# Kernel optimization log

Hardware: AMD Instinct MI355X
Metric: run time of the kernel (lower is better)

## Reference

```python
import jax, jax.numpy as jnp
import numpy as np
import functools

ISOVALUE = 0.0
OFFSET = 0.3  # quad half-extent used by the CPU fallback


def setup_inputs() -> dict:
    key = jax.random.key(0)
    k1, k2 = jax.random.split(key)
    grid = jax.random.normal(k1, (128, 128, 128), dtype=jnp.float32)
    deform = jax.random.normal(k2, (128, 128, 128, 3), dtype=jnp.float32)
    return {"grid": grid, "deform": deform}


def _mc_fallback(grid, deform):
    # Faithful, vectorized version of UniversalDiffMC.forward with the pure-CPU
    # fallback backend. Because JAX requires static shapes, we emit the dense
    # per-cell vertex/triangle buffers plus a validity mask instead of
    # compacting (inactive entries are zeroed).
    dimX, dimY, dimZ = grid.shape
    # F.pad(grid, (1,)*6, value=isovalue+1)
    gp = jnp.pad(grid, 1, constant_values=ISOVALUE + 1.0)        # [X+2,Y+2,Z+2]
    dp = jnp.pad(deform, ((1, 1), (1, 1), (1, 1), (0, 0)))       # [X+2,Y+2,Z+2,3]
    nx, ny, nz = dimX + 1, dimY + 1, dimZ + 1                    # cells of padded grid

    # 8 cube-corner values per cell via shifted slices
    def corner(dx, dy, dz):
        return gp[dx:dx + nx, dy:dy + ny, dz:dz + nz]
    corners = [corner(dx, dy, dz) for dx in (0, 1) for dy in (0, 1) for dz in (0, 1)]
    cmin = functools.reduce(jnp.minimum, corners)
    cmax = functools.reduce(jnp.maximum, corners)
    active = (cmin <= ISOVALUE) & (ISOVALUE <= cmax)             # [nx,ny,nz]

    # cell centers (x+0.5, y+0.5, z+0.5) + deform lookup at int(center)
    ix = jnp.arange(nx, dtype=grid.dtype)
    iy = jnp.arange(ny, dtype=grid.dtype)
    iz = jnp.arange(nz, dtype=grid.dtype)
    idx = jnp.stack(jnp.meshgrid(ix, iy, iz, indexing='ij'), axis=-1)  # [nx,ny,nz,3]
    center = idx + 0.5 + dp[:nx, :ny, :nz, :]                    # int(x+0.5)=x

    offs = jnp.array([[-OFFSET, -OFFSET, 0.0],
                      [ OFFSET, -OFFSET, 0.0],
                      [ OFFSET,  OFFSET, 0.0],
                      [-OFFSET,  OFFSET, 0.0]], dtype=grid.dtype)
    verts = center[..., None, :] + offs                          # [nx,ny,nz,4,3]
    verts = verts.reshape(-1, 3)

    # post-processing from forward(): shift back by padding, normalize to [-1,1)
    dims = jnp.array([dimX, dimY, dimZ], dtype=grid.dtype)
    verts = (verts - 1.0) / dims - 1.0

    mask_flat = active.reshape(-1)                                # [Ncells]
    vmask = jnp.repeat(mask_flat, 4)                              # [Ncells*4]
    verts = verts * vmask[:, None].astype(grid.dtype)

    ncells = nx * ny * nz
    base = jnp.arange(ncells, dtype=jnp.int32) * 4
    tri_pat = jnp.array([[0, 1, 2], [0, 2, 3]], dtype=jnp.int32)
    tris = (base[:, None, None] + tri_pat[None]).reshape(-1, 3)   # [Ncells*2,3]
    tmask = jnp.repeat(mask_flat, 2)
    tris = tris * tmask[:, None].astype(jnp.int32)
    return verts, tris, vmask


def reference(grid, deform):
    return _mc_fallback(grid, deform)
```

## Files before the change

kernel.cpp:

```cpp
#include <hip/hip_runtime.h>
#include <stdint.h>

constexpr int DIM    = 128;
constexpr int NCX    = 129;
constexpr int NCELLS = NCX * NCX * NCX;
constexpr size_t NV_ELEMS = (size_t)NCELLS * 12;
constexpr size_t NT_ELEMS = (size_t)NCELLS * 6;

constexpr int BLK = 256;

__device__ __forceinline__ float2 tri_pair(const float* __restrict__ smm,
                                           int c0, int j) {
    int cl = j / 3;
    int s  = j - 3 * cl;
    float mm = smm[cl];
    int base = (c0 + cl) * 4;
    int a = (s == 0) ? 0 : 2;
    int b = (s == 0) ? 1 : ((s == 1) ? 0 : 3);
    return make_float2((float)(base + a) * mm, (float)(base + b) * mm);
}

__global__ __launch_bounds__(BLK) void mc_kernel(
    const float* __restrict__ grid,
    const float* __restrict__ deform,
    float*       __restrict__ out)
{
    __shared__ __align__(16) float sv[BLK * 12];
    __shared__ float smm[BLK];

    const int t    = threadIdx.x;
    const int c0   = blockIdx.x * BLK;
    const int cell = c0 + t;

    if (cell < NCELLS) {
        int z  = cell % NCX;
        int tt = cell / NCX;
        int y  = tt % NCX;
        int x  = tt / NCX;

        float cmin = 3.4e38f, cmax = -3.4e38f;
        #pragma unroll
        for (int dx = 0; dx < 2; ++dx) {
            int i = x + dx - 1;
            bool iok = (unsigned)i < (unsigned)DIM;
            #pragma unroll
            for (int dy = 0; dy < 2; ++dy) {
                int j = y + dy - 1;
                bool jok = (unsigned)j < (unsigned)DIM;
                #pragma unroll
                for (int dz = 0; dz < 2; ++dz) {
                    int k = z + dz - 1;
                    bool kok = (unsigned)k < (unsigned)DIM;
                    float v = 1.0f;
                    if (iok && jok && kok)
                        v = grid[((size_t)i * DIM + j) * DIM + k];
                    cmin = fminf(cmin, v);
                    cmax = fmaxf(cmax, v);
                }
            }
        }
        float m = ((cmin <= 0.0f) && (cmax >= 0.0f)) ? 1.0f : 0.0f;

        float d0 = 0.f, d1 = 0.f, d2 = 0.f;
        {
            int i = x - 1, j = y - 1, k = z - 1;
            if ((unsigned)i < (unsigned)DIM && (unsigned)j < (unsigned)DIM &&
                (unsigned)k < (unsigned)DIM) {
                const float* b = deform + (((size_t)i * DIM + j) * DIM + k) * 3;
                d0 = b[0]; d1 = b[1]; d2 = b[2];
            }
        }
        float cx = (float)x + 0.5f + d0;
        float cy = (float)y + 0.5f + d1;
        float cz = (float)z + 0.5f + d2;

        constexpr float S = 1.0f / 128.0f;
        constexpr float B = -(1.0f / 128.0f) - 1.0f;
        float ax = fmaf(cx - 0.3f, S, B) * m;
        float bx = fmaf(cx + 0.3f, S, B) * m;
        float ay = fmaf(cy - 0.3f, S, B) * m;
        float by = fmaf(cy + 0.3f, S, B) * m;
        float gz = fmaf(cz,        S, B) * m;

        float4* v4 = reinterpret_cast<float4*>(sv) + t * 3;
        v4[0] = make_float4(ax, ay, gz, bx);
        v4[1] = make_float4(ay, gz, bx, by);
        v4[2] = make_float4(gz, ax, by, gz);

        smm[t] = m;
    }

    __syncthreads();

    float4*       gv  = reinterpret_cast<float4*>(out + (size_t)c0 * 12);
    const float4* lv  = reinterpret_cast<const float4*>(sv);
    float4*       gt4 = reinterpret_cast<float4*>(out + NV_ELEMS + (size_t)c0 * 6);
    float2*       gm  = reinterpret_cast<float2*>(out + NV_ELEMS + NT_ELEMS + (size_t)c0 * 4);

    if (c0 + BLK <= NCELLS) {
        #pragma unroll
        for (int r = 0; r < 3; ++r) gv[t + r * BLK] = lv[t + r * BLK];

        {
            float2 lo = tri_pair(smm, c0, 2 * t);
            float2 hi = tri_pair(smm, c0, 2 * t + 1);
            gt4[t] = make_float4(lo.x, lo.y, hi.x, hi.y);
            if (t < BLK / 2) {
                int p = BLK + t;
                float2 lo2 = tri_pair(smm, c0, 2 * p);
                float2 hi2 = tri_pair(smm, c0, 2 * p + 1);
                gt4[p] = make_float4(lo2.x, lo2.y, hi2.x, hi2.y);
            }
        }

        #pragma unroll
        for (int r = 0; r < 2; ++r) {
            int g = t + r * BLK;
            float mm = smm[g >> 1];
            gm[g] = make_float2(mm, mm);
        }
    } else {
        const int n = NCELLS - c0;
        for (int i = t; i < n * 3; i += BLK) gv[i] = lv[i];
        float2* gt2 = reinterpret_cast<float2*>(out + NV_ELEMS + (size_t)c0 * 6);
        for (int j = t; j < n * 3; j += BLK) gt2[j] = tri_pair(smm, c0, j);
        for (int g = t; g < n * 2; g += BLK) {
            float mm = smm[g >> 1];
            gm[g] = make_float2(mm, mm);
        }
    }
}

extern "C" void kernel_launch(void* const* d_in, const int* in_sizes, int n_in,
                              void* d_out, int out_size, void* d_ws, size_t ws_size,
                              hipStream_t stream) {
    const float* grid   = (const float*)d_in[0];
    const float* deform = (const float*)d_in[1];
    float* out = (float*)d_out;

    int blocks = (NCELLS + BLK - 1) / BLK;
    mc_kernel<<<blocks, BLK, 0, stream>>>(grid, deform, out);
}
```

Baseline: 39.94 us.

## Split vertex, triangle and mask output writes into separate block groups

The single kernel now dispatches three groups of blocks by block index: one writes vertices, one writes triangle indices, and one writes the vertex mask. The triangle and mask groups each recompute the cell activity mask from the grid. The aim is more blocks in flight, with each block writing one contiguous output region. The cost is that the 8-corner grid reads and min/max are done up to three times per cell.

```diff
diff --git a/kernel.cpp b/kernel.cpp
--- a/kernel.cpp
+++ b/kernel.cpp
@@ -8,6 +8,38 @@
 constexpr size_t NT_ELEMS = (size_t)NCELLS * 6;
 
 constexpr int BLK = 256;
+constexpr int NBV = (NCELLS + BLK - 1) / BLK;
+constexpr int NBT = NBV;
+constexpr int NBM = (NCELLS + 2 * BLK - 1) / (2 * BLK);
+
+__device__ __forceinline__ float cell_mask(const float* __restrict__ grid, int cell) {
+    int z  = cell % NCX;
+    int tt = cell / NCX;
+    int y  = tt % NCX;
+    int x  = tt / NCX;
+    float cmin = 3.4e38f, cmax = -3.4e38f;
+    #pragma unroll
+    for (int dx = 0; dx < 2; ++dx) {
+        int i = x + dx - 1;
+        bool iok = (unsigned)i < (unsigned)DIM;
+        #pragma unroll
+        for (int dy = 0; dy < 2; ++dy) {
+            int j = y + dy - 1;
+            bool jok = (unsigned)j < (unsigned)DIM;
+            #pragma unroll
+            for (int dz = 0; dz < 2; ++dz) {
+                int k = z + dz - 1;
+                bool kok = (unsigned)k < (unsigned)DIM;
+                float v = 1.0f;
+                if (iok && jok && kok)
+                    v = grid[((size_t)i * DIM + j) * DIM + k];
+                cmin = fminf(cmin, v);
+                cmax = fmaxf(cmax, v);
+            }
+        }
+    }
+    return ((cmin <= 0.0f) && (cmax >= 0.0f)) ? 1.0f : 0.0f;
+}
 
 __device__ __forceinline__ float2 tri_pair(const float* __restrict__ smm,
                                            int c0, int j) {
@@ -25,108 +57,102 @@
     const float* __restrict__ deform,
     float*       __restrict__ out)
 {
-    __shared__ __align__(16) float sv[BLK * 12];
-    __shared__ float smm[BLK];
+    __shared__ __align__(16) float sbuf[BLK * 12];
+    const int bid = blockIdx.x;
+    const int t   = threadIdx.x;
 
-    const int t    = threadIdx.x;
-    const int c0   = blockIdx.x * BLK;
-    const int cell = c0 + t;
+    if (bid < NBV) {
+        const int c0   = bid * BLK;
+        const int cell = c0 + t;
+        if (cell < NCELLS) {
+            int z  = cell % NCX;
+            int tt = cell / NCX;
+            int y  = tt % NCX;
+            int x  = tt / NCX;
+            float m = cell_mask(grid, cell);
 
-    if (cell < NCELLS) {
-        int z  = cell % NCX;
-        int tt = cell / NCX;
-        int y  = tt % NCX;
-        int x  = tt / NCX;
-
-        float cmin = 3.4e38f, cmax = -3.4e38f;
-        #pragma unroll
-        for (int dx = 0; dx < 2; ++dx) {
-            int i = x + dx - 1;
-            bool iok = (unsigned)i < (unsigned)DIM;
-            #pragma unroll
-            for (int dy = 0; dy < 2; ++dy) {
-                int j = y + dy - 1;
-                bool jok = (unsigned)j < (unsigned)DIM;
-                #pragma unroll
-                for (int dz = 0; dz < 2; ++dz) {
-                    int k = z + dz - 1;
-                    bool kok = (unsigned)k < (unsigned)DIM;
-                    float v = 1.0f;
-                    if (iok && jok && kok)
-                        v = grid[((size_t)i * DIM + j) * DIM + k];
-                    cmin = fminf(cmin, v);
-                    cmax = fmaxf(cmax, v);
-                }
-            }
-        }
-        float m = ((cmin <= 0.0f) && (cmax >= 0.0f)) ? 1.0f : 0.0f;
-
-        float d0 = 0.f, d1 = 0.f, d2 = 0.f;
-        {
+            float d0 = 0.f, d1 = 0.f, d2 = 0.f;
             int i = x - 1, j = y - 1, k = z - 1;
             if ((unsigned)i < (unsigned)DIM && (unsigned)j < (unsigned)DIM &&
                 (unsigned)k < (unsigned)DIM) {
                 const float* b = deform + (((size_t)i * DIM + j) * DIM + k) * 3;
                 d0 = b[0]; d1 = b[1]; d2 = b[2];
             }
+            float cx = (float)x + 0.5f + d0;
+            float cy = (float)y + 0.5f + d1;
+            float cz = (float)z + 0.5f + d2;
+
+            constexpr float S = 1.0f / 128.0f;
+            constexpr float B = -(1.0f / 128.0f) - 1.0f;
+            float ax = fmaf(cx - 0.3f, S, B) * m;
+            float bx = fmaf(cx + 0.3f, S, B) * m;
+            float ay = fmaf(cy - 0.3f, S, B) * m;
+            float by = fmaf(cy + 0.3f, S, B) * m;
+            float gz = fmaf(cz,        S, B) * m;
+
+            float4* v4 = reinterpret_cast<float4*>(sbuf) + t * 3;
+            v4[0] = make_float4(ax, ay, gz, bx);
+            v4[1] = make_float4(ay, gz, bx, by);
+            v4[2] = make_float4(gz, ax, by, gz);
         }
-        float cx = (float)x + 0.5f + d0;
-        float cy = (float)y + 0.5f + d1;
-        float cz = (float)z + 0.5f + d2;
+        __syncthreads();
 
-        constexpr float S = 1.0f / 128.0f;
-        constexpr float B = -(1.0f / 128.0f) - 1.0f;
-        float ax = fmaf(cx - 0.3f, S, B) * m;
-        float bx = fmaf(cx + 0.3f, S, B) * m;
-        float ay = fmaf(cy - 0.3f, S, B) * m;
-        float by = fmaf(cy + 0.3f, S, B) * m;
-        float gz = fmaf(cz,        S, B) * m;
+        float4*       gv = reinterpret_cast<float4*>(out + (size_t)c0 * 12);
+        const float4* lv = reinterpret_cast<const float4*>(sbuf);
+        if (c0 + BLK <= NCELLS) {
+            #pragma unroll
+            for (int r = 0; r < 3; ++r) gv[t + r * BLK] = lv[t + r * BLK];
+        } else {
+            const int n = NCELLS - c0;
+            for (int i2 = t; i2 < n * 3; i2 += BLK) gv[i2] = lv[i2];
+        }
 
-        float4* v4 = reinterpret_cast<float4*>(sv) + t * 3;
-        v4[0] = make_float4(ax, ay, gz, bx);
-        v4[1] = make_float4(ay, gz, bx, by);
-        v4[2] = make_float4(gz, ax, by, gz);
+    } else if (bid < NBV + NBT) {
+        const int c0   = (bid - NBV) * BLK;
+        const int cell = c0 + t;
+        sbuf[t] = (cell < NCELLS) ? cell_mask(grid, cell) : 0.0f;
+        __syncthreads();
 
-        smm[t] = m;
-    }
-
-    __syncthreads();
-
-    float4*       gv  = reinterpret_cast<float4*>(out + (size_t)c0 * 12);
-    const float4* lv  = reinterpret_cast<const float4*>(sv);
-    float4*       gt4 = reinterpret_cast<float4*>(out + NV_ELEMS + (size_t)c0 * 6);
-    float2*       gm  = reinterpret_cast<float2*>(out + NV_ELEMS + NT_ELEMS + (size_t)c0 * 4);
-
-    if (c0 + BLK <= NCELLS) {
-        #pragma unroll
-        for (int r = 0; r < 3; ++r) gv[t + r * BLK] = lv[t + r * BLK];
-
-        {
-            float2 lo = tri_pair(smm, c0, 2 * t);
-            float2 hi = tri_pair(smm, c0, 2 * t + 1);
+        if (c0 + BLK <= NCELLS) {
+            float4* gt4 = reinterpret_cast<float4*>(out + NV_ELEMS + (size_t)c0 * 6);
+            float2 lo = tri_pair(sbuf, c0, 2 * t);
+            float2 hi = tri_pair(sbuf, c0, 2 * t + 1);
             gt4[t] = make_float4(lo.x, lo.y, hi.x, hi.y);
             if (t < BLK / 2) {
                 int p = BLK + t;
-                float2 lo2 = tri_pair(smm, c0, 2 * p);
-                float2 hi2 = tri_pair(smm, c0, 2 * p + 1);
+                float2 lo2 = tri_pair(sbuf, c0, 2 * p);
+                float2 hi2 = tri_pair(sbuf, c0, 2 * p + 1);
                 gt4[p] = make_float4(lo2.x, lo2.y, hi2.x, hi2.y);
             }
+        } else {
+            const int n = NCELLS - c0;
+            float2* gt2 = reinterpret_cast<float2*>(out + NV_ELEMS + (size_t)c0 * 6);
+            for (int j = t; j < n * 3; j += BLK) gt2[j] = tri_pair(sbuf, c0, j);
         }
 
+    } else {
+        const int c0 = (bid - NBV - NBT) * (2 * BLK);
         #pragma unroll
         for (int r = 0; r < 2; ++r) {
-            int g = t + r * BLK;
-            float mm = smm[g >> 1];
-            gm[g] = make_float2(mm, mm);
+            int cell = c0 + t + r * BLK;
+            sbuf[t + r * BLK] = (cell < NCELLS) ? cell_mask(grid, cell) : 0.0f;
         }
-    } else {
-        const int n = NCELLS - c0;
-        for (int i = t; i < n * 3; i += BLK) gv[i] = lv[i];
-        float2* gt2 = reinterpret_cast<float2*>(out + NV_ELEMS + (size_t)c0 * 6);
-        for (int j = t; j < n * 3; j += BLK) gt2[j] = tri_pair(smm, c0, j);
-        for (int g = t; g < n * 2; g += BLK) {
-            float mm = smm[g >> 1];
-            gm[g] = make_float2(mm, mm);
+        __syncthreads();
+
+        float2* gm = reinterpret_cast<float2*>(out + NV_ELEMS + NT_ELEMS + (size_t)c0 * 4);
+        const int n = min(2 * BLK, NCELLS - c0);
+        if (n == 2 * BLK) {
+            #pragma unroll
+            for (int r = 0; r < 4; ++r) {
+                int g = t + r * BLK;
+                float mm = sbuf[g >> 1];
+                gm[g] = make_float2(mm, mm);
+            }
+        } else {
+            for (int g = t; g < n * 2; g += BLK) {
+                float mm = sbuf[g >> 1];
+                gm[g] = make_float2(mm, mm);
+            }
         }
     }
 }
@@ -138,6 +164,6 @@
     const float* deform = (const float*)d_in[1];
     float* out = (float*)d_out;
 
-    int blocks = (NCELLS + BLK - 1) / BLK;
+    int blocks = NBV + NBT + NBM;
     mc_kernel<<<blocks, BLK, 0, stream>>>(grid, deform, out);
 }
```

Result: slower. 45.25 us (+13.3%).
